# Performance work log

Hardware: AMD Instinct MI355X
Metric: run time of the kernel (lower is better)

## Reference

```python
import jax, jax.numpy as jnp
import numpy as np

N = 100000
E = 1600000


def seg_softmax(alpha, dst, n):
    # numerically stable softmax over variable-size destination segments
    amax = jax.ops.segment_max(alpha, dst, num_segments=n)
    amax = jnp.where(jnp.isfinite(amax), amax, 0.0)
    ex = jnp.exp(alpha - amax[dst])
    denom = jax.ops.segment_sum(ex, dst, num_segments=n)
    return ex / (denom[dst] + 1e-16)


def setup_inputs() -> dict:
    key = jax.random.key(0)
    ks = jax.random.split(key, 24)
    p = lambda k, shape: (jax.random.normal(k, shape, jnp.float32) * 0.1)
    x = jax.random.normal(ks[0], (N, 3), jnp.float32)
    edge_index = jax.random.randint(ks[1], (2, E), 0, N, dtype=jnp.int64)
    return {
        'x': x, 'edge_index': edge_index,
        # GATConv(3,16,heads=4): shared lin (no bias), att_src/att_dst, final bias
        'W1': p(ks[2], (3, 64)), 'att_src1': p(ks[3], (4, 16)), 'att_dst1': p(ks[4], (4, 16)), 'b1': jnp.zeros((64,), jnp.float32),
        # GATv2Conv(64,16,heads=2): lin_l, lin_r (both with bias), att, final bias
        'W2l': p(ks[5], (64, 32)), 'b2l': jnp.zeros((32,), jnp.float32),
        'W2r': p(ks[6], (64, 32)), 'b2r': jnp.zeros((32,), jnp.float32),
        'att2': p(ks[7], (2, 16)), 'b2': jnp.zeros((32,), jnp.float32),
        # TransformerConv(32,7,heads=1): q/k/v lins + skip lin (all with bias)
        'Wq': p(ks[8], (32, 7)), 'bq': jnp.zeros((7,), jnp.float32),
        'Wk': p(ks[9], (32, 7)), 'bk': jnp.zeros((7,), jnp.float32),
        'Wv': p(ks[10], (32, 7)), 'bv': jnp.zeros((7,), jnp.float32),
        'Wskip': p(ks[11], (32, 7)), 'bskip': jnp.zeros((7,), jnp.float32),
    }


def reference(x, edge_index, W1, att_src1, att_dst1, b1, W2l, b2l, W2r, b2r, att2, b2,
              Wq, bq, Wk, bk, Wv, bv, Wskip, bskip):
    n = x.shape[0]
    loop = jnp.arange(n, dtype=edge_index.dtype)
    # edge index with self-loops (GATConv / GATv2Conv default add_self_loops=True)
    src = jnp.concatenate([edge_index[0], loop])
    dst = jnp.concatenate([edge_index[1], loop])

    # ---- layer 1: GATConv(3, 16, heads=4) ----
    h = (x @ W1).reshape(n, 4, 16)                       # [N,H,C]
    a_src = (h * att_src1[None]).sum(-1)                 # [N,H]
    a_dst = (h * att_dst1[None]).sum(-1)
    alpha = jax.nn.leaky_relu(a_src[src] + a_dst[dst], 0.2)  # [E+N,H]
    alpha = seg_softmax(alpha, dst, n)
    out = jax.ops.segment_sum(h[src] * alpha[..., None], dst, num_segments=n)
    x1 = jax.nn.relu(out.reshape(n, 64) + b1)

    # ---- layer 2: GATv2Conv(64, 16, heads=2) ----
    hl = (x1 @ W2l + b2l).reshape(n, 2, 16)
    hr = (x1 @ W2r + b2r).reshape(n, 2, 16)
    e = jax.nn.leaky_relu(hl[src] + hr[dst], 0.2)        # [E+N,H,C]
    alpha = (e * att2[None]).sum(-1)                     # [E+N,H]
    alpha = seg_softmax(alpha, dst, n)
    out = jax.ops.segment_sum(hl[src] * alpha[..., None], dst, num_segments=n)
    x2 = out.reshape(n, 32) + b2

    # ---- layer 3: TransformerConv(32, 7, heads=1); no self-loops by default ----
    s, d = edge_index[0], edge_index[1]
    q = x2 @ Wq + bq                                     # [N,7] (H=1,C=7)
    k = x2 @ Wk + bk
    v = x2 @ Wv + bv
    scale = 1.0 / jnp.sqrt(jnp.float32(7.0))
    alpha = (q[d] * k[s]).sum(-1) * scale                # [E]
    alpha = seg_softmax(alpha, d, n)
    out = jax.ops.segment_sum(v[s] * alpha[:, None], d, num_segments=n)
    x3 = out + (x2 @ Wskip + bskip)                      # root_weight skip connection
    return x3
```

## Files before the change

### kernel.cpp

```cpp
#include <hip/hip_runtime.h>
#include <hip/hip_bf16.h>

typedef __hip_bfloat16 bf16;

static __device__ __forceinline__ float us2f(unsigned short u) {
    union { unsigned int i; float f; } c; c.i = ((unsigned int)u) << 16; return c.f;
}
static __device__ __forceinline__ unsigned short f2us(float f) {
    union { float f; unsigned int i; } c; c.f = f;
    unsigned int r = c.i + 0x7FFF + ((c.i >> 16) & 1);
    return (unsigned short)(r >> 16);
}


__global__ __launch_bounds__(256) void k_detect(const unsigned short* __restrict__ xr,
                                                const int* __restrict__ er,
                                                int* __restrict__ flags) {
    __shared__ int sbad, snz;
    int tid = threadIdx.x;
    if (tid == 0) { sbad = 0; snz = 0; }
    __syncthreads();
    int bad = 0, nz = 0;
    for (int i = tid; i < 1024; i += 256) {
        unsigned short w = xr[2 * i];
        int ex = (w >> 7) & 0xFF;
        if (ex < 110 || ex > 135) bad++;
        if (er[2 * i + 1] != 0) nz++;
    }
    atomicAdd(&sbad, bad);
    atomicAdd(&snz, nz);
    __syncthreads();
    if (tid == 0) {
        flags[0] = (sbad > 256) ? 1 : 0;
        flags[1] = (snz < 512) ? 1 : 0;
    }
}

struct CvtArgs { const void* p[19]; int sz[19]; };

__global__ __launch_bounds__(256) void k_convert(CvtArgs a, const int* __restrict__ flags,
                                                 float* __restrict__ dst, int total) {
    int t = blockIdx.x * 256 + threadIdx.x;
    if (t >= total) return;
    int isf32 = flags[0];
    int base = 0, seg = -1, off = 0;
#pragma unroll
    for (int i = 0; i < 19; i++) {
        if (seg < 0 && t < base + a.sz[i]) { seg = i; off = t - base; }
        base += a.sz[i];
    }
    const void* p = a.p[seg];
    float v = isf32 ? ((const float*)p)[off] : __bfloat162float(((const bf16*)p)[off]);
    dst[t] = v;
}

static __device__ __forceinline__ int ld_edge(const int* er, size_t i, int idx64) {
    return idx64 ? er[2 * i] : er[i];
}


__global__ __launch_bounds__(1024) void k_bscatter(const int* __restrict__ er, const int* __restrict__ flags,
                                                   int* __restrict__ bcur, int2* __restrict__ bkt,
                                                   int E, int NB, int C) {
    __shared__ int cnt[256];
    __shared__ int res[256];
    int tid = threadIdx.x;
    if (tid < 256) cnt[tid] = 0;
    __syncthreads();
    int idx64 = flags[1];
    int base = blockIdx.x * 4096 + tid;
    int sv[4], dv[4], bv[4];
    bool val[4];
#pragma unroll
    for (int k = 0; k < 4; ++k) {
        int e = base + k * 1024;
        val[k] = (e < E);
        if (val[k]) {
            sv[k] = ld_edge(er, (size_t)e, idx64);
            dv[k] = ld_edge(er, (size_t)E + e, idx64);
            bv[k] = dv[k] >> 10;
            atomicAdd(&cnt[bv[k]], 1);
        }
    }
    __syncthreads();
    if (tid < NB) {
        int c = cnt[tid];
        res[tid] = c ? atomicAdd(&bcur[tid], c) : 0;
        cnt[tid] = 0;
    }
    __syncthreads();
#pragma unroll
    for (int k = 0; k < 4; ++k) {
        if (val[k]) {
            int r = res[bv[k]] + atomicAdd(&cnt[bv[k]], 1);
            if (r < C) bkt[(size_t)bv[k] * C + r] = make_int2(sv[k], dv[k]);
        }
    }
}

__global__ __launch_bounds__(1024) void k_bbuild(const int2* __restrict__ bkt, const int* __restrict__ bcur,
                                                 int2* __restrict__ off2, int* __restrict__ csr, int N, int C) {
    __shared__ int sm[1024];
    int b = blockIdx.x, tid = threadIdx.x;
    int node0 = b << 10;
    size_t base = (size_t)b * C;
    int m = bcur[b]; if (m > C) m = C;
    sm[tid] = 0;
    __syncthreads();
    const int2* bp = bkt + base;
    for (int i = tid; i < m; i += 1024) atomicAdd(&sm[bp[i].y - node0], 1);
    __syncthreads();
    int v = sm[tid];
    for (int d = 1; d < 1024; d <<= 1) {
        int t = (tid >= d) ? sm[tid - d] : 0;
        __syncthreads();
        sm[tid] += t;
        __syncthreads();
    }
    int excl = sm[tid] - v;
    int node = node0 + tid;
    if (node < N) off2[node] = make_int2((int)base + excl, (int)base + excl + v);
    __syncthreads();
    sm[tid] = excl;
    __syncthreads();
    for (int i = tid; i < m; i += 1024) {
        int2 sd = bp[i];
        int r = atomicAdd(&sm[sd.y - node0], 1);
        csr[base + r] = sd.x;
    }
}


__global__ __launch_bounds__(256) void k_l1_transform(const float* __restrict__ x, const float* __restrict__ W1,
                                                      const float* __restrict__ att_s, const float* __restrict__ att_d,
                                                      float4* __restrict__ x4, float* __restrict__ as1,
                                                      float* __restrict__ ad1, int N) {
    int tid = threadIdx.x;
    int node = blockIdx.x * 4 + (tid >> 6);
    if (node >= N) return;
    int lane = tid & 63;
    float x0 = x[node * 3 + 0];
    float x1 = x[node * 3 + 1];
    float x2 = x[node * 3 + 2];
    float h = x0 * W1[lane] + x1 * W1[64 + lane] + x2 * W1[128 + lane];
    if (lane == 0) x4[node] = make_float4(x0, x1, x2, 0.f);
    float ts = h * att_s[lane];
    float td = h * att_d[lane];
    for (int m = 8; m >= 1; m >>= 1) { ts += __shfl_xor(ts, m); td += __shfl_xor(td, m); }
    if ((lane & 15) == 0) {
        as1[node * 4 + (lane >> 4)] = ts;
        ad1[node * 4 + (lane >> 4)] = td;
    }
}

__global__ __launch_bounds__(256) void k_l1_agg(const float4* __restrict__ x4, const float4* __restrict__ as4,
                                                const float4* __restrict__ ad4p, const int2* __restrict__ off2,
                                                const int* __restrict__ csr, const float* __restrict__ W1,
                                                const float* __restrict__ b1,
                                                float* __restrict__ x1, int N) {
    int tid = threadIdx.x;
    int node = blockIdx.x * 16 + (tid >> 4);
    if (node >= N) return;
    int sl = tid & 15;
    int lane = tid & 63;
    int lb = lane & 48;

    float4 ad = ad4p[node];
    int2 ee = off2[node];
    int e0 = ee.x, e1 = ee.y;

    float v[16];
#pragma unroll
    for (int i = 0; i < 16; ++i) v[i] = 0.f;

    for (int jj = e0 + sl; jj < e1; jj += 16) {
        int s = csr[jj];
        float4 a = as4[s];
        float4 xv = x4[s];
        float z0 = a.x + ad.x, z1 = a.y + ad.y, z2 = a.z + ad.z, z3 = a.w + ad.w;
        z0 = (z0 > 0.f) ? z0 : 0.2f * z0;
        z1 = (z1 > 0.f) ? z1 : 0.2f * z1;
        z2 = (z2 > 0.f) ? z2 : 0.2f * z2;
        z3 = (z3 > 0.f) ? z3 : 0.2f * z3;
        float w0 = __expf(z0), w1 = __expf(z1), w2 = __expf(z2), w3 = __expf(z3);
        v[0] += w0 * xv.x; v[1] += w0 * xv.y; v[2]  += w0 * xv.z; v[3]  += w0;
        v[4] += w1 * xv.x; v[5] += w1 * xv.y; v[6]  += w1 * xv.z; v[7]  += w1;
        v[8] += w2 * xv.x; v[9] += w2 * xv.y; v[10] += w2 * xv.z; v[11] += w2;
        v[12] += w3 * xv.x; v[13] += w3 * xv.y; v[14] += w3 * xv.z; v[15] += w3;
    }

#pragma unroll
    for (int d = 8; d >= 1; d >>= 1) {
#pragma unroll
        for (int i = 0; i < 16; ++i) {
            if (i < d) {
                float a = v[i], b = v[i + d];
                float send = (sl & d) ? a : b;
                float recv = __shfl_xor(send, d);
                v[i] = ((sl & d) ? b : a) + recv;
            }
        }
    }
    float r = v[0];

    float agx[4], agy[4], agz[4], dn[4];
#pragma unroll
    for (int h = 0; h < 4; ++h) {
        agx[h] = __shfl(r, lb + 4 * h + 0);
        agy[h] = __shfl(r, lb + 4 * h + 1);
        agz[h] = __shfl(r, lb + 4 * h + 2);
        dn[h]  = __shfl(r, lb + 4 * h + 3);
    }

    {
        float4 a = as4[node];
        float4 xv = x4[node];
        float z0 = a.x + ad.x, z1 = a.y + ad.y, z2 = a.z + ad.z, z3 = a.w + ad.w;
        z0 = (z0 > 0.f) ? z0 : 0.2f * z0;
        z1 = (z1 > 0.f) ? z1 : 0.2f * z1;
        z2 = (z2 > 0.f) ? z2 : 0.2f * z2;
        z3 = (z3 > 0.f) ? z3 : 0.2f * z3;
        float w0 = __expf(z0), w1 = __expf(z1), w2 = __expf(z2), w3 = __expf(z3);
        agx[0] += w0 * xv.x; agy[0] += w0 * xv.y; agz[0] += w0 * xv.z; dn[0] += w0;
        agx[1] += w1 * xv.x; agy[1] += w1 * xv.y; agz[1] += w1 * xv.z; dn[1] += w1;
        agx[2] += w2 * xv.x; agy[2] += w2 * xv.y; agz[2] += w2 * xv.z; dn[2] += w2;
        agx[3] += w3 * xv.x; agy[3] += w3 * xv.y; agz[3] += w3 * xv.z; dn[3] += w3;
    }

#pragma unroll
    for (int h = 0; h < 4; ++h) {
        int j = h * 16 + sl;
        float inv = 1.f / (dn[h] + 1e-16f);
        float o = (agx[h] * W1[j] + agy[h] * W1[64 + j] + agz[h] * W1[128 + j]) * inv + b1[j];
        x1[(size_t)node * 64 + j] = (o > 0.f) ? o : 0.f;
    }
}


__global__ __launch_bounds__(256) void k_l2_transform(const float* __restrict__ x1,
                                                      const float* __restrict__ W2l, const float* __restrict__ b2l,
                                                      const float* __restrict__ W2r, const float* __restrict__ b2r,
                                                      unsigned short* __restrict__ hlb, float* __restrict__ hr, int N) {
    __shared__ float xs[64 * 68];
    int t = threadIdx.x;
    int node0 = blockIdx.x * 64;
    int nrem = N - node0; if (nrem > 64) nrem = 64;
    const float4* xg = (const float4*)x1;
#pragma unroll
    for (int it = 0; it < 4; ++it) {
        int id = it * 256 + t;
        int row = id >> 4, c4 = id & 15;
        float4 v = make_float4(0.f, 0.f, 0.f, 0.f);
        if (row < nrem) v = xg[(size_t)(node0 + row) * 16 + c4];
        *(float4*)&xs[row * 68 + c4 * 4] = v;
    }
    __syncthreads();
    int nt = t >> 4;
    int jt = t & 15;
    int jq = jt & 7;
    int jc = jq * 4;
    const float4* W4 = (const float4*)((jt < 8) ? W2l : W2r);
    const float4* B4 = (const float4*)((jt < 8) ? b2l : b2r);
    float4 bb = B4[jq];
    float4 acc[4];
#pragma unroll
    for (int i = 0; i < 4; ++i) acc[i] = bb;
#pragma unroll 2
    for (int k4 = 0; k4 < 16; ++k4) {
        float4 w0 = W4[(k4 * 4 + 0) * 8 + jq];
        float4 w1 = W4[(k4 * 4 + 1) * 8 + jq];
        float4 w2 = W4[(k4 * 4 + 2) * 8 + jq];
        float4 w3 = W4[(k4 * 4 + 3) * 8 + jq];
#pragma unroll
        for (int i = 0; i < 4; ++i) {
            float4 xv = *(const float4*)&xs[(nt + i * 16) * 68 + k4 * 4];
            acc[i].x += xv.x * w0.x + xv.y * w1.x + xv.z * w2.x + xv.w * w3.x;
            acc[i].y += xv.x * w0.y + xv.y * w1.y + xv.z * w2.y + xv.w * w3.y;
            acc[i].z += xv.x * w0.z + xv.y * w1.z + xv.z * w2.z + xv.w * w3.z;
            acc[i].w += xv.x * w0.w + xv.y * w1.w + xv.z * w2.w + xv.w * w3.w;
        }
    }
#pragma unroll
    for (int i = 0; i < 4; ++i) {
        int row = nt + i * 16;
        if (row < nrem) {
            size_t node = node0 + row;
            if (jt < 8) {
                uint2 p;
                p.x = (unsigned)f2us(acc[i].x) | ((unsigned)f2us(acc[i].y) << 16);
                p.y = (unsigned)f2us(acc[i].z) | ((unsigned)f2us(acc[i].w) << 16);
                *(uint2*)&hlb[node * 32 + jc] = p;
            } else {
                *(float4*)&hr[node * 32 + jc] = acc[i];
            }
        }
    }
}

__global__ __launch_bounds__(256) void k_l2_agg(const unsigned short* __restrict__ hlb, const float* __restrict__ hr,
                                                const float* __restrict__ att2, const float* __restrict__ b2,
                                                const int2* __restrict__ off2, const int* __restrict__ csr,
                                                float* __restrict__ x2, int N) {
    int tid = threadIdx.x;
    int node = blockIdx.x * 16 + (tid >> 4);
    if (node >= N) return;
    int sl = tid & 15;

    float hrd[32];
    {
        const float4* hr4 = (const float4*)(hr + (size_t)node * 32);
#pragma unroll
        for (int q = 0; q < 8; ++q) {
            float4 v = hr4[q];
            hrd[4 * q + 0] = v.x; hrd[4 * q + 1] = v.y;
            hrd[4 * q + 2] = v.z; hrd[4 * q + 3] = v.w;
        }
    }

    float accA[16], accB[16];
#pragma unroll
    for (int i = 0; i < 16; ++i) { accA[i] = 0.f; accB[i] = 0.f; }
    float den0 = 0.f, den1 = 0.f;

    int2 ee = off2[node];
    int e0 = ee.x, e1 = ee.y;
    for (int jj = e0 + sl; jj < e1; jj += 16) {
        int s = csr[jj];
        const uint4* hp = (const uint4*)(hlb + (size_t)s * 32);
        uint4 u0 = hp[0], u1 = hp[1], u2 = hp[2], u3 = hp[3];
        unsigned int uu[16] = {u0.x, u0.y, u0.z, u0.w, u1.x, u1.y, u1.z, u1.w,
                               u2.x, u2.y, u2.z, u2.w, u3.x, u3.y, u3.z, u3.w};
        float t0 = 0.f, t1 = 0.f;
#pragma unroll
        for (int q = 0; q < 8; ++q) {
            float lo = __uint_as_float(uu[q] << 16);
            float hi = __uint_as_float(uu[q] & 0xFFFF0000u);
            float el = lo + hrd[2 * q];     el = fmaxf(el, 0.2f * el);
            float eh = hi + hrd[2 * q + 1]; eh = fmaxf(eh, 0.2f * eh);
            t0 += att2[2 * q] * el + att2[2 * q + 1] * eh;
        }
#pragma unroll
        for (int q = 8; q < 16; ++q) {
            float lo = __uint_as_float(uu[q] << 16);
            float hi = __uint_as_float(uu[q] & 0xFFFF0000u);
            float el = lo + hrd[2 * q];     el = fmaxf(el, 0.2f * el);
            float eh = hi + hrd[2 * q + 1]; eh = fmaxf(eh, 0.2f * eh);
            t1 += att2[2 * q] * el + att2[2 * q + 1] * eh;
        }
        float w0 = __expf(t0), w1 = __expf(t1);
        den0 += w0; den1 += w1;
#pragma unroll
        for (int q = 0; q < 8; ++q) {
            accA[2 * q]     += w0 * __uint_as_float(uu[q] << 16);
            accA[2 * q + 1] += w0 * __uint_as_float(uu[q] & 0xFFFF0000u);
        }
#pragma unroll
        for (int q = 8; q < 16; ++q) {
            accB[2 * (q - 8)]     += w1 * __uint_as_float(uu[q] << 16);
            accB[2 * (q - 8) + 1] += w1 * __uint_as_float(uu[q] & 0xFFFF0000u);
        }
    }

#pragma unroll
    for (int d = 8; d >= 1; d >>= 1) {
#pragma unroll
        for (int i = 0; i < 16; ++i) {
            if (i < d) {
                { float a = accA[i], b = accA[i + d];
                  float send = (sl & d) ? a : b;
                  float recv = __shfl_xor(send, d);
                  accA[i] = ((sl & d) ? b : a) + recv; }
                { float a = accB[i], b = accB[i + d];
                  float send = (sl & d) ? a : b;
                  float recv = __shfl_xor(send, d);
                  accB[i] = ((sl & d) ? b : a) + recv; }
            }
        }
        den0 += __shfl_xor(den0, d);
        den1 += __shfl_xor(den1, d);
    }
    float sumA = accA[0];
    float sumB = accB[0];

    float hr0 = hr[(size_t)node * 32 + sl];
    float hr1 = hr[(size_t)node * 32 + 16 + sl];
    float hl0 = us2f(hlb[(size_t)node * 32 + sl]);
    float hl1 = us2f(hlb[(size_t)node * 32 + 16 + sl]);
    float ea = hl0 + hr0; ea = fmaxf(ea, 0.2f * ea);
    float eb = hl1 + hr1; eb = fmaxf(eb, 0.2f * eb);
    float p0 = att2[sl] * ea;
    float p1 = att2[16 + sl] * eb;
    p0 += __shfl_xor(p0, 1); p0 += __shfl_xor(p0, 2); p0 += __shfl_xor(p0, 4); p0 += __shfl_xor(p0, 8);
    p1 += __shfl_xor(p1, 1); p1 += __shfl_xor(p1, 2); p1 += __shfl_xor(p1, 4); p1 += __shfl_xor(p1, 8);
    float w0 = __expf(p0), w1 = __expf(p1);
    sumA += w0 * hl0; den0 += w0;
    sumB += w1 * hl1; den1 += w1;

    x2[(size_t)node * 32 + sl]      = sumA / (den0 + 1e-16f) + b2[sl];
    x2[(size_t)node * 32 + 16 + sl] = sumB / (den1 + 1e-16f) + b2[16 + sl];
}


__global__ __launch_bounds__(1024) void k_l3_wcat(const float* __restrict__ Wq, const float* __restrict__ bq,
                                                  const float* __restrict__ Wk, const float* __restrict__ bk,
                                                  const float* __restrict__ Wv, const float* __restrict__ bv,
                                                  const float* __restrict__ Ws, const float* __restrict__ bs,
                                                  float* __restrict__ Wcat, float* __restrict__ bcat) {
    int t = threadIdx.x;
    int c = t & 31, g = c >> 3, cc = c & 7;
    const float* Wg = (g == 0) ? Wq : (g == 1) ? Ws : (g == 2) ? Wk : Wv;
    const float* Bg = (g == 0) ? bq : (g == 1) ? bs : (g == 2) ? bk : bv;
    int kk = t >> 5;
    Wcat[t] = (cc < 7) ? Wg[kk * 7 + cc] : 0.f;
    if (t < 32) bcat[t] = (cc < 7) ? Bg[cc] : 0.f;
}

__global__ __launch_bounds__(256) void k_l3_transform(const float* __restrict__ x2,
                                                      const float4* __restrict__ Wc4, const float4* __restrict__ bc4,
                                                      float* __restrict__ QS, float* __restrict__ KV, int N) {
    __shared__ float xs[128 * 36];
    int t = threadIdx.x;
    int node0 = blockIdx.x * 128;
    int nrem = N - node0; if (nrem > 128) nrem = 128;
    const float4* xg = (const float4*)x2;
#pragma unroll
    for (int it = 0; it < 4; ++it) {
        int id = it * 256 + t;
        int row = id >> 3, c4 = id & 7;
        float4 v = make_float4(0.f, 0.f, 0.f, 0.f);
        if (row < nrem) v = xg[(size_t)(node0 + row) * 8 + c4];
        *(float4*)&xs[row * 36 + c4 * 4] = v;
    }
    __syncthreads();
    int nt = t >> 3;
    int jt = t & 7;
    float4 bb = bc4[jt];
    float4 acc[4];
#pragma unroll
    for (int i = 0; i < 4; ++i) acc[i] = bb;
#pragma unroll 2
    for (int k4 = 0; k4 < 8; ++k4) {
        float4 w0 = Wc4[(k4 * 4 + 0) * 8 + jt];
        float4 w1 = Wc4[(k4 * 4 + 1) * 8 + jt];
        float4 w2 = Wc4[(k4 * 4 + 2) * 8 + jt];
        float4 w3 = Wc4[(k4 * 4 + 3) * 8 + jt];
#pragma unroll
        for (int i = 0; i < 4; ++i) {
            float4 xv = *(const float4*)&xs[(nt + i * 32) * 36 + k4 * 4];
            acc[i].x += xv.x * w0.x + xv.y * w1.x + xv.z * w2.x + xv.w * w3.x;
            acc[i].y += xv.x * w0.y + xv.y * w1.y + xv.z * w2.y + xv.w * w3.y;
            acc[i].z += xv.x * w0.z + xv.y * w1.z + xv.z * w2.z + xv.w * w3.z;
            acc[i].w += xv.x * w0.w + xv.y * w1.w + xv.z * w2.w + xv.w * w3.w;
        }
    }
#pragma unroll
    for (int i = 0; i < 4; ++i) {
        int row = nt + i * 32;
        if (row < nrem) {
            size_t node = node0 + row;
            float* dst = (jt < 4) ? (QS + node * 16 + jt * 4) : (KV + node * 16 + (jt - 4) * 4);
            *(float4*)dst = acc[i];
        }
    }
}

__global__ __launch_bounds__(256) void k_l3_agg(const float* __restrict__ QS, const float* __restrict__ KV,
                                                const int2* __restrict__ off2, const int* __restrict__ csr,
                                                float* __restrict__ out, int N) {
    int tid = threadIdx.x;
    int node = blockIdx.x * 32 + (tid >> 3);
    if (node >= N) return;
    int sl = tid & 7;
    int lane = tid & 63;
    const float scale = 0.3779644730092272f;
    const float4* q4 = (const float4*)(QS + (size_t)node * 16);
    float4 qa = q4[0], qb = q4[1];
    qa.x *= scale; qa.y *= scale; qa.z *= scale; qa.w *= scale;
    qb.x *= scale; qb.y *= scale; qb.z *= scale; qb.w = 0.f;

    float v[8];
#pragma unroll
    for (int i = 0; i < 8; ++i) v[i] = 0.f;

    int2 ee = off2[node];
    int e0 = ee.x, e1 = ee.y;
    for (int jj = e0 + sl; jj < e1; jj += 8) {
        int s = csr[jj];
        const float4* kp = (const float4*)(KV + (size_t)s * 16);
        float4 k0 = kp[0], k1 = kp[1], v0 = kp[2], v1 = kp[3];
        float t = qa.x * k0.x + qa.y * k0.y + qa.z * k0.z + qa.w * k0.w
                + qb.x * k1.x + qb.y * k1.y + qb.z * k1.z;
        float w = __expf(t);
        v[0] += w * v0.x; v[1] += w * v0.y; v[2] += w * v0.z; v[3] += w * v0.w;
        v[4] += w * v1.x; v[5] += w * v1.y; v[6] += w * v1.z; v[7] += w;
    }
#pragma unroll
    for (int d = 4; d >= 1; d >>= 1) {
#pragma unroll
        for (int i = 0; i < 8; ++i) {
            if (i < d) {
                float a = v[i], b = v[i + d];
                float send = (sl & d) ? a : b;
                float recv = __shfl_xor(send, d);
                v[i] = ((sl & d) ? b : a) + recv;
            }
        }
    }
    float r = v[0];
    float den = __shfl(r, (lane & 56) + 7);
    if (sl < 7) out[(size_t)node * 7 + sl] = r / (den + 1e-16f)
                                             + QS[(size_t)node * 16 + 8 + sl];
}


extern "C" void kernel_launch(void* const* d_in, const int* in_sizes, int n_in,
                              void* d_out, int out_size, void* d_ws, size_t ws_size,
                              hipStream_t stream) {
    const int* ei = (const int*)d_in[1];
    float* out = (float*)d_out;

    int N = in_sizes[0] / 3;
    int E = in_sizes[1] / 2;
    int NB = (N + 1023) >> 10;
    int C = (E + NB - 1) / NB + 4096;

    char* ws = (char*)d_ws;
    size_t o = 0;
    auto take = [&](size_t bytes) -> char* {
        char* p = ws + o;
        o = (o + bytes + 255) & ~(size_t)255;
        return p;
    };
    int*   flags   = (int*)take(64);
    int total_f = 0;
    for (int i = 0; i < 20; ++i) if (i != 1) total_f += in_sizes[i];
    float* canon   = (float*)take((size_t)total_f * 4);
    float* Wcat    = (float*)take(32 * 32 * 4);
    float* bcat    = (float*)take(32 * 4);
    int2*  off2    = (int2*)take((size_t)N * 8);
    int*   bcur    = (int*)take(256 * 4);
    int*   csr     = (int*)take((size_t)NB * C * 4);
    float* bufA    = (float*)take((size_t)N * 64 * 4);
    float* as1     = (float*)take((size_t)N * 4 * 4);
    float* ad1     = (float*)take((size_t)N * 4 * 4);
    float* bufB    = (float*)take((size_t)N * 64 * 4);
    (void)ws_size; (void)n_in; (void)out_size;

    CvtArgs ca;
    const float* cp[20];
    {
        int off_ = 0, k = 0;
        for (int i = 0; i < 20; ++i) {
            if (i == 1) { cp[i] = nullptr; continue; }
            ca.p[k] = d_in[i];
            ca.sz[k] = in_sizes[i];
            cp[i] = canon + off_;
            off_ += in_sizes[i];
            ++k;
        }
    }

    hipMemsetAsync(bcur, 0, 256 * 4, stream);
    k_detect<<<1, 256, 0, stream>>>((const unsigned short*)d_in[0], ei, flags);
    k_convert<<<(total_f + 255) / 256, 256, 0, stream>>>(ca, flags, canon, total_f);
    k_l3_wcat<<<1, 1024, 0, stream>>>(cp[12], cp[13], cp[14], cp[15], cp[16], cp[17],
                                      cp[18], cp[19], Wcat, bcat);

    int2* bkt = (int2*)bufB;
    int gb = (E + 4095) / 4096;
    k_bscatter<<<gb, 1024, 0, stream>>>(ei, flags, bcur, bkt, E, NB, C);
    k_bbuild<<<NB, 1024, 0, stream>>>(bkt, bcur, off2, csr, N, C);

    float4* x4 = (float4*)bufA;
    k_l1_transform<<<(N + 3) / 4, 256, 0, stream>>>(cp[0], cp[2], cp[3], cp[4], x4, as1, ad1, N);
    float* x1 = bufB;
    k_l1_agg<<<(N + 15) / 16, 256, 0, stream>>>(x4, (const float4*)as1, (const float4*)ad1,
                                                off2, csr, cp[2], cp[5], x1, N);

    unsigned short* hlb = (unsigned short*)bufA;
    float* hr = bufA + (size_t)N * 16;
    k_l2_transform<<<(N + 63) / 64, 256, 0, stream>>>(x1, cp[6], cp[7], cp[8], cp[9], hlb, hr, N);
    float* x2 = bufB;
    k_l2_agg<<<(N + 15) / 16, 256, 0, stream>>>(hlb, hr, cp[10], cp[11], off2, csr, x2, N);

    float* QS = bufA;
    float* KV = bufA + (size_t)N * 16;
    k_l3_transform<<<(N + 127) / 128, 256, 0, stream>>>(x2, (const float4*)Wcat, (const float4*)bcat,
                                                        QS, KV, N);
    k_l3_agg<<<(N + 31) / 32, 256, 0, stream>>>(QS, KV, off2, csr, out, N);
}
```

Measured before the change: 289.8 us.

## Fold detect and weight-concat kernels into convert, pack bucket entries into one int

Removes the separate k_detect and k_l3_wcat launches. Each convert and scatter block now probes the dtype and index-width flags itself, and an extra convert block builds Wcat/bcat. Bucket entries shrink from int2 (src,dst) to a single int packing src<<10 with the low 10 bits of dst, which halves the scatter/build traffic. The risks are redundant probe reads in every block and overflow of the packed encoding if source ids exceed 2^21.

```diff
diff --git a/kernel.cpp b/kernel.cpp
--- a/kernel.cpp
+++ b/kernel.cpp
@@ -12,73 +12,96 @@
     return (unsigned short)(r >> 16);
 }
 
-
-__global__ __launch_bounds__(256) void k_detect(const unsigned short* __restrict__ xr,
-                                                const int* __restrict__ er,
-                                                int* __restrict__ flags) {
-    __shared__ int sbad, snz;
-    int tid = threadIdx.x;
-    if (tid == 0) { sbad = 0; snz = 0; }
-    __syncthreads();
-    int bad = 0, nz = 0;
-    for (int i = tid; i < 1024; i += 256) {
-        unsigned short w = xr[2 * i];
-        int ex = (w >> 7) & 0xFF;
-        if (ex < 110 || ex > 135) bad++;
-        if (er[2 * i + 1] != 0) nz++;
-    }
-    atomicAdd(&sbad, bad);
-    atomicAdd(&snz, nz);
-    __syncthreads();
-    if (tid == 0) {
-        flags[0] = (sbad > 256) ? 1 : 0;
-        flags[1] = (snz < 512) ? 1 : 0;
-    }
-}
+static __device__ __forceinline__ int probe_isf32(const unsigned short* xr, int* sflag) {
+    int tid = threadIdx.x;
+    if (tid < 64) {
+        int bad = 0;
+        for (int i = tid; i < 1024; i += 64) {
+            int ex = (xr[2 * i] >> 7) & 0xFF;
+            if (ex < 110 || ex > 135) bad++;
+        }
+#pragma unroll
+        for (int m = 32; m >= 1; m >>= 1) bad += __shfl_xor(bad, m);
+        if (tid == 0) *sflag = (bad > 256) ? 1 : 0;
+    }
+    __syncthreads();
+    return *sflag;
+}
+
+static __device__ __forceinline__ int ld_edge(const int* er, size_t i, int idx64) {
+    return idx64 ? er[2 * i] : er[i];
+}
+
 
 struct CvtArgs { const void* p[19]; int sz[19]; };
 
-__global__ __launch_bounds__(256) void k_convert(CvtArgs a, const int* __restrict__ flags,
-                                                 float* __restrict__ dst, int total) {
-    int t = blockIdx.x * 256 + threadIdx.x;
+static __device__ __forceinline__ float cvt_elem(const void* p, int off, int isf32) {
+    return isf32 ? ((const float*)p)[off] : __bfloat162float(((const bf16*)p)[off]);
+}
+
+__global__ __launch_bounds__(256) void k_convert(CvtArgs a, float* __restrict__ dst, int total,
+                                                 int nbconv, float* __restrict__ Wcat,
+                                                 float* __restrict__ bcat) {
+    __shared__ int sflag;
+    int isf32 = probe_isf32((const unsigned short*)a.p[0], &sflag);
+    int tid = threadIdx.x;
+    if ((int)blockIdx.x == nbconv) {
+#pragma unroll
+        for (int t4 = 0; t4 < 4; ++t4) {
+            int idx = t4 * 256 + tid;
+            int c = idx & 31, g = c >> 3, cc = c & 7, kk = idx >> 5;
+            const void* Wg = (g == 0) ? a.p[11] : (g == 1) ? a.p[17] : (g == 2) ? a.p[13] : a.p[15];
+            Wcat[idx] = (cc < 7) ? cvt_elem(Wg, kk * 7 + cc, isf32) : 0.f;
+        }
+        if (tid < 32) {
+            int g = tid >> 3, cc = tid & 7;
+            const void* Bg = (g == 0) ? a.p[12] : (g == 1) ? a.p[18] : (g == 2) ? a.p[14] : a.p[16];
+            bcat[tid] = (cc < 7) ? cvt_elem(Bg, cc, isf32) : 0.f;
+        }
+        return;
+    }
+    int t = blockIdx.x * 256 + tid;
     if (t >= total) return;
-    int isf32 = flags[0];
     int base = 0, seg = -1, off = 0;
 #pragma unroll
     for (int i = 0; i < 19; i++) {
         if (seg < 0 && t < base + a.sz[i]) { seg = i; off = t - base; }
         base += a.sz[i];
     }
-    const void* p = a.p[seg];
-    float v = isf32 ? ((const float*)p)[off] : __bfloat162float(((const bf16*)p)[off]);
-    dst[t] = v;
-}
-
-static __device__ __forceinline__ int ld_edge(const int* er, size_t i, int idx64) {
-    return idx64 ? er[2 * i] : er[i];
-}
-
-
-__global__ __launch_bounds__(1024) void k_bscatter(const int* __restrict__ er, const int* __restrict__ flags,
-                                                   int* __restrict__ bcur, int2* __restrict__ bkt,
+    dst[t] = cvt_elem(a.p[seg], off, isf32);
+}
+
+
+__global__ __launch_bounds__(1024) void k_bscatter(const int* __restrict__ er,
+                                                   int* __restrict__ bcur, int* __restrict__ bkt,
                                                    int E, int NB, int C) {
     __shared__ int cnt[256];
     __shared__ int res[256];
-    int tid = threadIdx.x;
+    __shared__ int sflag;
+    int tid = threadIdx.x;
+    if (tid < 64) {
+        int lim = (E < 1024) ? E : 1024;
+        int nz = 0;
+        for (int i = tid; i < lim; i += 64) if (er[2 * i + 1] != 0) nz++;
+#pragma unroll
+        for (int m = 32; m >= 1; m >>= 1) nz += __shfl_xor(nz, m);
+        if (tid == 0) sflag = (nz < ((E < 1024 ? E : 1024) >> 1)) ? 1 : 0;
+    }
     if (tid < 256) cnt[tid] = 0;
     __syncthreads();
-    int idx64 = flags[1];
+    int idx64 = sflag;
     int base = blockIdx.x * 4096 + tid;
-    int sv[4], dv[4], bv[4];
+    int pk[4], bv[4];
     bool val[4];
 #pragma unroll
     for (int k = 0; k < 4; ++k) {
         int e = base + k * 1024;
         val[k] = (e < E);
         if (val[k]) {
-            sv[k] = ld_edge(er, (size_t)e, idx64);
-            dv[k] = ld_edge(er, (size_t)E + e, idx64);
-            bv[k] = dv[k] >> 10;
+            int s = ld_edge(er, (size_t)e, idx64);
+            int d = ld_edge(er, (size_t)E + e, idx64);
+            bv[k] = d >> 10;
+            pk[k] = (s << 10) | (d & 1023);
             atomicAdd(&cnt[bv[k]], 1);
         }
     }
@@ -93,22 +116,21 @@
     for (int k = 0; k < 4; ++k) {
         if (val[k]) {
             int r = res[bv[k]] + atomicAdd(&cnt[bv[k]], 1);
-            if (r < C) bkt[(size_t)bv[k] * C + r] = make_int2(sv[k], dv[k]);
-        }
-    }
-}
-
-__global__ __launch_bounds__(1024) void k_bbuild(const int2* __restrict__ bkt, const int* __restrict__ bcur,
+            if (r < C) bkt[(size_t)bv[k] * C + r] = pk[k];
+        }
+    }
+}
+
+__global__ __launch_bounds__(1024) void k_bbuild(const int* __restrict__ bkt, const int* __restrict__ bcur,
                                                  int2* __restrict__ off2, int* __restrict__ csr, int N, int C) {
     __shared__ int sm[1024];
     int b = blockIdx.x, tid = threadIdx.x;
-    int node0 = b << 10;
     size_t base = (size_t)b * C;
     int m = bcur[b]; if (m > C) m = C;
     sm[tid] = 0;
     __syncthreads();
-    const int2* bp = bkt + base;
-    for (int i = tid; i < m; i += 1024) atomicAdd(&sm[bp[i].y - node0], 1);
+    const int* bp = bkt + base;
+    for (int i = tid; i < m; i += 1024) atomicAdd(&sm[bp[i] & 1023], 1);
     __syncthreads();
     int v = sm[tid];
     for (int d = 1; d < 1024; d <<= 1) {
@@ -118,15 +140,15 @@
         __syncthreads();
     }
     int excl = sm[tid] - v;
-    int node = node0 + tid;
+    int node = (b << 10) + tid;
     if (node < N) off2[node] = make_int2((int)base + excl, (int)base + excl + v);
     __syncthreads();
     sm[tid] = excl;
     __syncthreads();
     for (int i = tid; i < m; i += 1024) {
-        int2 sd = bp[i];
-        int r = atomicAdd(&sm[sd.y - node0], 1);
-        csr[base + r] = sd.x;
+        int p = bp[i];
+        int r = atomicAdd(&sm[p & 1023], 1);
+        csr[base + r] = p >> 10;
     }
 }
 
@@ -401,20 +423,6 @@
 }
 
 
-__global__ __launch_bounds__(1024) void k_l3_wcat(const float* __restrict__ Wq, const float* __restrict__ bq,
-                                                  const float* __restrict__ Wk, const float* __restrict__ bk,
-                                                  const float* __restrict__ Wv, const float* __restrict__ bv,
-                                                  const float* __restrict__ Ws, const float* __restrict__ bs,
-                                                  float* __restrict__ Wcat, float* __restrict__ bcat) {
-    int t = threadIdx.x;
-    int c = t & 31, g = c >> 3, cc = c & 7;
-    const float* Wg = (g == 0) ? Wq : (g == 1) ? Ws : (g == 2) ? Wk : Wv;
-    const float* Bg = (g == 0) ? bq : (g == 1) ? bs : (g == 2) ? bk : bv;
-    int kk = t >> 5;
-    Wcat[t] = (cc < 7) ? Wg[kk * 7 + cc] : 0.f;
-    if (t < 32) bcat[t] = (cc < 7) ? Bg[cc] : 0.f;
-}
-
 __global__ __launch_bounds__(256) void k_l3_transform(const float* __restrict__ x2,
                                                       const float4* __restrict__ Wc4, const float4* __restrict__ bc4,
                                                       float* __restrict__ QS, float* __restrict__ KV, int N) {
@@ -531,7 +539,6 @@
         o = (o + bytes + 255) & ~(size_t)255;
         return p;
     };
-    int*   flags   = (int*)take(64);
     int total_f = 0;
     for (int i = 0; i < 20; ++i) if (i != 1) total_f += in_sizes[i];
     float* canon   = (float*)take((size_t)total_f * 4);
@@ -561,14 +568,12 @@
     }
 
     hipMemsetAsync(bcur, 0, 256 * 4, stream);
-    k_detect<<<1, 256, 0, stream>>>((const unsigned short*)d_in[0], ei, flags);
-    k_convert<<<(total_f + 255) / 256, 256, 0, stream>>>(ca, flags, canon, total_f);
-    k_l3_wcat<<<1, 1024, 0, stream>>>(cp[12], cp[13], cp[14], cp[15], cp[16], cp[17],
-                                      cp[18], cp[19], Wcat, bcat);
-
-    int2* bkt = (int2*)bufB;
+    int nbconv = (total_f + 255) / 256;
+    k_convert<<<nbconv + 1, 256, 0, stream>>>(ca, canon, total_f, nbconv, Wcat, bcat);
+
+    int* bkt = (int*)bufB;
     int gb = (E + 4095) / 4096;
-    k_bscatter<<<gb, 1024, 0, stream>>>(ei, flags, bcur, bkt, E, NB, C);
+    k_bscatter<<<gb, 1024, 0, stream>>>(ei, bcur, bkt, E, NB, C);
     k_bbuild<<<NB, 1024, 0, stream>>>(bkt, bcur, off2, csr, N, C);
 
     float4* x4 = (float4*)bufA;
```

Result: faster. 279.5 us (-3.6%).
